# Optimization experiments

Hardware: AMD Instinct MI355X
Metric: run time of the kernel (lower is better)

The kernel has to match this reference:

```python
import jax, jax.numpy as jnp
import numpy as np

S, C, HF, WF = 6, 64, 44, 80          # cameras, feat channels, feat H, feat W
H_IMG, W_IMG = 352.0, 640.0           # full image size (opt.height/opt.width)
Z, Y, X = 16, 100, 100                # voxel grid (opt.voxels_size)
XMIN, XMAX = -40.0, 40.0
YMIN, YMAX = -40.0, 40.0
ZMIN, ZMAX = -1.0, 5.4
EPS = 1e-6


def setup_inputs() -> dict:
    key = jax.random.key(0)
    features = jax.random.normal(jax.random.fold_in(key, 0), (S, C, HF, WF), dtype=jnp.float32)
    # intrinsics at full image resolution
    K = np.eye(4, dtype=np.float32)
    K[0, 0] = 500.0; K[1, 1] = 500.0
    K[0, 2] = W_IMG / 2.0; K[1, 2] = H_IMG / 2.0
    pix_T_cams = np.tile(K[None], (S, 1, 1))
    # 6-camera surround rig: cam0_T_camX rigid transforms (columns = camera axes in ref frame)
    mats = []
    for i in range(S):
        th = 2.0 * np.pi * i / S
        c, s = np.cos(th), np.sin(th)
        T = np.eye(4, dtype=np.float32)
        T[:3, 0] = [-s, c, 0.0]          # camera x (right)
        T[:3, 1] = [0.0, 0.0, -1.0]      # camera y (down)
        T[:3, 2] = [c, s, 0.0]           # camera z (forward)
        T[:3, 3] = [0.5 * c, 0.5 * s, 1.5]
        mats.append(T)
    cam0_T_camXs = np.stack(mats).astype(np.float32)
    return {"features": features,
            "pix_T_cams": jnp.asarray(pix_T_cams),
            "cam0_T_camXs": jnp.asarray(cam0_T_camXs)}


def _safe_inverse(T):
    # rigid 4x4 inverse: [R t] -> [R^T, -R^T t]
    R = T[:, :3, :3]
    t = T[:, :3, 3]
    Rt = jnp.swapaxes(R, 1, 2)
    tt = -jnp.einsum('sij,sj->si', Rt, t)
    inv = jnp.zeros_like(T)
    inv = inv.at[:, :3, :3].set(Rt).at[:, :3, 3].set(tt).at[:, 3, 3].set(1.0)
    return inv


def _voxel_centers():
    # ref-frame coordinates of voxel centers, flattened [Z*Y*X, 3] with x fastest
    vx = (XMAX - XMIN) / X
    vy = (YMAX - YMIN) / Y
    vz = (ZMAX - ZMIN) / Z
    xs = XMIN + vx * (jnp.arange(X, dtype=jnp.float32) + 0.5)
    ys = YMIN + vy * (jnp.arange(Y, dtype=jnp.float32) + 0.5)
    zs = ZMIN + vz * (jnp.arange(Z, dtype=jnp.float32) + 0.5)
    zz, yy, xx = jnp.meshgrid(zs, ys, xs, indexing='ij')
    return jnp.stack([xx, yy, zz], axis=-1).reshape(-1, 3)


def _bilinear(img, x, y):
    # img: [C,H,W]; x,y: [N] pixel coords; zero padding outside
    Hh, Ww = img.shape[-2], img.shape[-1]
    x0 = jnp.floor(x)
    y0 = jnp.floor(y)
    wx1 = x - x0
    wy1 = y - y0

    def corner(xi, yi, w):
        valid = (xi >= 0) & (xi < Ww) & (yi >= 0) & (yi < Hh)
        xc = jnp.clip(xi, 0, Ww - 1).astype(jnp.int32)
        yc = jnp.clip(yi, 0, Hh - 1).astype(jnp.int32)
        return img[:, yc, xc] * (w * valid)[None, :]

    return (corner(x0, y0, (1 - wx1) * (1 - wy1))
            + corner(x0 + 1, y0, wx1 * (1 - wy1))
            + corner(x0, y0 + 1, (1 - wx1) * wy1)
            + corner(x0 + 1, y0 + 1, wx1 * wy1))  # [C,N]


def reference(features, pix_T_cams, cam0_T_camXs):
    camXs_T_cam0 = _safe_inverse(cam0_T_camXs)
    sx, sy = WF / W_IMG, HF / H_IMG
    scale = jnp.diag(jnp.array([sx, sy, 1.0, 1.0], jnp.float32))
    featpix_T_cams = jnp.einsum('ij,sjk->sik', scale, pix_T_cams)
    pix_T_cam0 = jnp.einsum('sij,sjk->sik', featpix_T_cams, camXs_T_cam0)

    xyz0 = _voxel_centers()                                  # [N,3]
    xyz1 = jnp.concatenate([xyz0, jnp.ones((xyz0.shape[0], 1), jnp.float32)], -1)
    xyz_pix = jnp.einsum('sij,nj->sni', pix_T_cam0, xyz1)    # [S,N,4]
    z_cam = jnp.einsum('sj,nj->sn', camXs_T_cam0[:, 2, :], xyz1)  # camX-frame depth

    denom = jnp.maximum(xyz_pix[..., 2], 1e-6)
    x_pix = xyz_pix[..., 0] / denom
    y_pix = xyz_pix[..., 1] / denom
    valid = ((x_pix > -0.5) & (x_pix < WF - 0.5)
             & (y_pix > -0.5) & (y_pix < HF - 0.5)
             & (z_cam > 0.0))

    # grid_sample(align_corners=False) with norm 2*(p/W)-1 samples at pixel p-0.5
    samp = jax.vmap(_bilinear)(features, x_pix - 0.5, y_pix - 0.5)  # [S,C,N]
    feat_mems = samp * valid[:, None, :].astype(samp.dtype)
    feat_mems = feat_mems.reshape(S, C, Z, Y, X)[None]              # [1,S,C,Z,Y,X]

    mask = (jnp.abs(feat_mems) > 0).astype(feat_mems.dtype)
    feat_mem = (feat_mems * mask).sum(1) / (mask.sum(1) + EPS)      # masked mean over cams
    return jnp.transpose(feat_mem, (0, 1, 4, 3, 2))                 # [1,C,X,Y,Z]
```

## Files before the change

### kernel.cpp

```cpp
#include <hip/hip_runtime.h>

#define NS 6
#define NC 64
#define HF 44
#define WF 80
#define HW (HF * WF)
#define NZ 16
#define NY 100
#define NX 100
#define XYZ (NX * NY * NZ)

__global__ __launch_bounds__(256) void transpose_feat(
        const float* __restrict__ in, float* __restrict__ outT) {
    __shared__ float tile[64 * 65];
    int b = blockIdx.x;
    int s = b / 55;
    int hw0 = (b % 55) * 64;
    int t = threadIdx.x;
#pragma unroll
    for (int i = 0; i < 16; ++i) {
        int e = t + i * 256;
        int c = e >> 6, w = e & 63;
        tile[c * 65 + w] = in[((size_t)(s * NC + c)) * HW + hw0 + w];
    }
    __syncthreads();
#pragma unroll
    for (int i = 0; i < 16; ++i) {
        int e = t + i * 256;
        int hwl = e >> 6, c = e & 63;
        outT[((size_t)s * HW + hw0 + hwl) * NC + c] = tile[c * 65 + hwl];
    }
}

template <bool TRANS>
__global__ __launch_bounds__(256) void volpool(
        const float* __restrict__ feat,
        const float* __restrict__ pix,
        const float* __restrict__ c0TX,
        float* __restrict__ out) {
    __shared__ float  mlds[NS * 16];
    __shared__ float4 wts[96];
    __shared__ int4   offs[96];
    __shared__ int    vflags[96];
    __shared__ float  ostage[NC * 17];

    int t = threadIdx.x;
    int b = blockIdx.x;
    int x = b % NX, y = b / NX;

    if (t < NS) {
        const float* T = c0TX + t * 16;
        float inv[4][4];
        for (int i = 0; i < 3; ++i) {
            for (int j = 0; j < 3; ++j) inv[i][j] = T[j * 4 + i];
            inv[i][3] = -(T[0 * 4 + i] * T[0 * 4 + 3] +
                          T[1 * 4 + i] * T[1 * 4 + 3] +
                          T[2 * 4 + i] * T[2 * 4 + 3]);
        }
        inv[3][0] = 0.f; inv[3][1] = 0.f; inv[3][2] = 0.f; inv[3][3] = 1.f;
        const float sx = (float)WF / 640.0f;
        const float sy = (float)HF / 352.0f;
        const float* K = pix + t * 16;
        float fp[3][4];
        for (int j = 0; j < 4; ++j) {
            fp[0][j] = sx * K[0 * 4 + j];
            fp[1][j] = sy * K[1 * 4 + j];
            fp[2][j] = K[2 * 4 + j];
        }
        float* M = mlds + t * 16;
        for (int i = 0; i < 3; ++i)
            for (int j = 0; j < 4; ++j) {
                float acc = 0.f;
                for (int k = 0; k < 4; ++k) acc += fp[i][k] * inv[k][j];
                M[i * 4 + j] = acc;
            }
        for (int j = 0; j < 4; ++j) M[12 + j] = inv[2][j];
    }
    __syncthreads();

    if (t < 96) {
        int s = t % NS, z = t / NS;
        const float* M = mlds + s * 16;
        float xw = -40.0f + 0.8f * ((float)x + 0.5f);
        float yw = -40.0f + 0.8f * ((float)y + 0.5f);
        float zw = -1.0f + 0.4f * ((float)z + 0.5f);
        float px = M[0] * xw + M[1] * yw + M[2]  * zw + M[3];
        float py = M[4] * xw + M[5] * yw + M[6]  * zw + M[7];
        float pz = M[8] * xw + M[9] * yw + M[10] * zw + M[11];
        float zc = M[12] * xw + M[13] * yw + M[14] * zw + M[15];
        float denom = fmaxf(pz, 1e-6f);
        float xp = px / denom, yp = py / denom;
        bool valid = (xp > -0.5f) & (xp < (float)WF - 0.5f) &
                     (yp > -0.5f) & (yp < (float)HF - 0.5f) & (zc > 0.0f);
        vflags[t] = valid ? 1 : 0;
        if (valid) {
            float xs = xp - 0.5f, ys = yp - 0.5f;
            float x0f = floorf(xs), y0f = floorf(ys);
            float wx1 = xs - x0f, wy1 = ys - y0f;
            float wx0 = 1.f - wx1, wy0 = 1.f - wy1;
            int x0 = (int)x0f, y0 = (int)y0f;
            int x1 = x0 + 1, y1 = y0 + 1;
            bool bx0 = (x0 >= 0) & (x0 < WF);
            bool bx1 = (x1 >= 0) & (x1 < WF);
            bool by0 = (y0 >= 0) & (y0 < HF);
            bool by1 = (y1 >= 0) & (y1 < HF);
            int x0c = min(max(x0, 0), WF - 1);
            int x1c = min(max(x1, 0), WF - 1);
            int y0c = min(max(y0, 0), HF - 1);
            int y1c = min(max(y1, 0), HF - 1);
            float4 w;
            w.x = wx0 * wy0 * (float)(bx0 & by0);
            w.y = wx1 * wy0 * (float)(bx1 & by0);
            w.z = wx0 * wy1 * (float)(bx0 & by1);
            w.w = wx1 * wy1 * (float)(bx1 & by1);
            int p00 = y0c * WF + x0c, p10 = y0c * WF + x1c;
            int p01 = y1c * WF + x0c, p11 = y1c * WF + x1c;
            int4 o;
            if (TRANS) {
                o.x = (s * HW + p00) * NC;
                o.y = (s * HW + p10) * NC;
                o.z = (s * HW + p01) * NC;
                o.w = (s * HW + p11) * NC;
            } else {
                o.x = s * NC * HW + p00;
                o.y = s * NC * HW + p10;
                o.z = s * NC * HW + p01;
                o.w = s * NC * HW + p11;
            }
            wts[t] = w;
            offs[t] = o;
        }
    }
    __syncthreads();

    int cg = t & 15, z = t >> 4;
    float4 sum = make_float4(0.f, 0.f, 0.f, 0.f);
    float4 cnt = make_float4(0.f, 0.f, 0.f, 0.f);
    for (int s = 0; s < NS; ++s) {
        int idx = z * NS + s;
        if (!vflags[idx]) continue;
        float4 w = wts[idx];
        int4 o = offs[idx];
        float4 f00, f10, f01, f11;
        if (TRANS) {
            int ch4 = cg << 2;
            f00 = *(const float4*)(feat + o.x + ch4);
            f10 = *(const float4*)(feat + o.y + ch4);
            f01 = *(const float4*)(feat + o.z + ch4);
            f11 = *(const float4*)(feat + o.w + ch4);
        } else {
            int c0 = cg << 2;
            f00.x = feat[o.x + (c0 + 0) * HW]; f00.y = feat[o.x + (c0 + 1) * HW];
            f00.z = feat[o.x + (c0 + 2) * HW]; f00.w = feat[o.x + (c0 + 3) * HW];
            f10.x = feat[o.y + (c0 + 0) * HW]; f10.y = feat[o.y + (c0 + 1) * HW];
            f10.z = feat[o.y + (c0 + 2) * HW]; f10.w = feat[o.y + (c0 + 3) * HW];
            f01.x = feat[o.z + (c0 + 0) * HW]; f01.y = feat[o.z + (c0 + 1) * HW];
            f01.z = feat[o.z + (c0 + 2) * HW]; f01.w = feat[o.z + (c0 + 3) * HW];
            f11.x = feat[o.w + (c0 + 0) * HW]; f11.y = feat[o.w + (c0 + 1) * HW];
            f11.z = feat[o.w + (c0 + 2) * HW]; f11.w = feat[o.w + (c0 + 3) * HW];
        }
        float vx = w.x * f00.x + w.y * f10.x + w.z * f01.x + w.w * f11.x;
        float vy = w.x * f00.y + w.y * f10.y + w.z * f01.y + w.w * f11.y;
        float vz = w.x * f00.z + w.y * f10.z + w.z * f01.z + w.w * f11.z;
        float vw = w.x * f00.w + w.y * f10.w + w.z * f01.w + w.w * f11.w;
        sum.x += vx; cnt.x += (vx != 0.0f) ? 1.0f : 0.0f;
        sum.y += vy; cnt.y += (vy != 0.0f) ? 1.0f : 0.0f;
        sum.z += vz; cnt.z += (vz != 0.0f) ? 1.0f : 0.0f;
        sum.w += vw; cnt.w += (vw != 0.0f) ? 1.0f : 0.0f;
    }
    int c0 = cg << 2;
    ostage[(c0 + 0) * 17 + z] = sum.x / (cnt.x + 1e-6f);
    ostage[(c0 + 1) * 17 + z] = sum.y / (cnt.y + 1e-6f);
    ostage[(c0 + 2) * 17 + z] = sum.z / (cnt.z + 1e-6f);
    ostage[(c0 + 3) * 17 + z] = sum.w / (cnt.w + 1e-6f);
    __syncthreads();

    int c = t >> 2, zq = t & 3;
    float4 v4;
    v4.x = ostage[c * 17 + zq * 4 + 0];
    v4.y = ostage[c * 17 + zq * 4 + 1];
    v4.z = ostage[c * 17 + zq * 4 + 2];
    v4.w = ostage[c * 17 + zq * 4 + 3];
    float* o = out + (size_t)c * XYZ + ((size_t)x * NY + y) * NZ + zq * 4;
    *(float4*)o = v4;
}

extern "C" void kernel_launch(void* const* d_in, const int* in_sizes, int n_in,
                              void* d_out, int out_size, void* d_ws, size_t ws_size,
                              hipStream_t stream) {
    const float* features = (const float*)d_in[0];
    const float* pix      = (const float*)d_in[1];
    const float* c0TX     = (const float*)d_in[2];
    float* out   = (float*)d_out;
    float* featT = (float*)d_ws;
    size_t need = sizeof(float) * (size_t)NS * HW * NC;

    if (ws_size >= need) {
        hipLaunchKernelGGL(transpose_feat, dim3(NS * 55), dim3(256), 0, stream,
                           features, featT);
        hipLaunchKernelGGL((volpool<true>), dim3(NX * NY), dim3(256), 0, stream,
                           featT, pix, c0TX, out);
    } else {
        hipLaunchKernelGGL((volpool<false>), dim3(NX * NY), dim3(256), 0, stream,
                           features, pix, c0TX, out);
    }
}
```

Baseline: 87.59 us.

## Vectorize transpose, compact valid cameras, remap blocks, and use nontemporal stores

The transpose kernel now moves float4 chunks per thread instead of scalars. The pooling kernel builds a compacted per-z list of valid cameras so the gather loop skips invalid entries, and it software-pipelines the feature loads by prefetching the next camera's corners. Block indices are remapped into 8 spatial regions so that concurrently running blocks spread across the grid. Output writes use nontemporal stores to avoid polluting the cache. These changes add an extra sync phase and more register pressure.

```diff
diff --git a/kernel.cpp b/kernel.cpp
--- a/kernel.cpp
+++ b/kernel.cpp
@@ -10,6 +10,8 @@
 #define NX 100
 #define XYZ (NX * NY * NZ)
 
+typedef float v4f __attribute__((ext_vector_type(4)));
+
 __global__ __launch_bounds__(256) void transpose_feat(
         const float* __restrict__ in, float* __restrict__ outT) {
     __shared__ float tile[64 * 65];
@@ -18,17 +20,26 @@
     int hw0 = (b % 55) * 64;
     int t = threadIdx.x;
 #pragma unroll
-    for (int i = 0; i < 16; ++i) {
+    for (int i = 0; i < 4; ++i) {
         int e = t + i * 256;
-        int c = e >> 6, w = e & 63;
-        tile[c * 65 + w] = in[((size_t)(s * NC + c)) * HW + hw0 + w];
+        int c = e >> 4, wg = e & 15;
+        float4 f = *(const float4*)(in + ((size_t)(s * NC + c)) * HW + hw0 + wg * 4);
+        tile[c * 65 + wg * 4 + 0] = f.x;
+        tile[c * 65 + wg * 4 + 1] = f.y;
+        tile[c * 65 + wg * 4 + 2] = f.z;
+        tile[c * 65 + wg * 4 + 3] = f.w;
     }
     __syncthreads();
 #pragma unroll
-    for (int i = 0; i < 16; ++i) {
+    for (int i = 0; i < 4; ++i) {
         int e = t + i * 256;
-        int hwl = e >> 6, c = e & 63;
-        outT[((size_t)s * HW + hw0 + hwl) * NC + c] = tile[c * 65 + hwl];
+        int hwl = e >> 4, cg = e & 15;
+        float4 f;
+        f.x = tile[(cg * 4 + 0) * 65 + hwl];
+        f.y = tile[(cg * 4 + 1) * 65 + hwl];
+        f.z = tile[(cg * 4 + 2) * 65 + hwl];
+        f.w = tile[(cg * 4 + 3) * 65 + hwl];
+        *(float4*)(outT + ((size_t)s * HW + hw0 + hwl) * NC + cg * 4) = f;
     }
 }
 
@@ -42,11 +53,16 @@
     __shared__ float4 wts[96];
     __shared__ int4   offs[96];
     __shared__ int    vflags[96];
+    __shared__ int    vidx[NZ][NS];
+    __shared__ int    nvalid[NZ];
     __shared__ float  ostage[NC * 17];
 
     int t = threadIdx.x;
     int b = blockIdx.x;
-    int x = b % NX, y = b / NX;
+    int reg = b & 7;
+    int r = b >> 3;
+    int x = (reg & 1) * 50 + (r % 50);
+    int y = (reg >> 1) * 25 + (r / 50);
 
     if (t < NS) {
         const float* T = c0TX + t * 16;
@@ -133,56 +149,96 @@
     }
     __syncthreads();
 
+    if (t < NZ) {
+        int n = 0;
+        for (int s = 0; s < NS; ++s) {
+            int idx = t * NS + s;
+            if (vflags[idx]) vidx[t][n++] = idx;
+        }
+        nvalid[t] = n;
+    }
+    __syncthreads();
+
     int cg = t & 15, z = t >> 4;
+    int ch4 = cg << 2;
     float4 sum = make_float4(0.f, 0.f, 0.f, 0.f);
     float4 cnt = make_float4(0.f, 0.f, 0.f, 0.f);
-    for (int s = 0; s < NS; ++s) {
-        int idx = z * NS + s;
-        if (!vflags[idx]) continue;
-        float4 w = wts[idx];
-        int4 o = offs[idx];
-        float4 f00, f10, f01, f11;
+    int nv = nvalid[z];
+    if (nv > 0) {
         if (TRANS) {
-            int ch4 = cg << 2;
-            f00 = *(const float4*)(feat + o.x + ch4);
-            f10 = *(const float4*)(feat + o.y + ch4);
-            f01 = *(const float4*)(feat + o.z + ch4);
-            f11 = *(const float4*)(feat + o.w + ch4);
+            int idx = vidx[z][0];
+            float4 w = wts[idx];
+            int4 o = offs[idx];
+            float4 f00 = *(const float4*)(feat + o.x + ch4);
+            float4 f10 = *(const float4*)(feat + o.y + ch4);
+            float4 f01 = *(const float4*)(feat + o.z + ch4);
+            float4 f11 = *(const float4*)(feat + o.w + ch4);
+            for (int j = 1; j < nv; ++j) {
+                int idx2 = vidx[z][j];
+                float4 w2 = wts[idx2];
+                int4 o2 = offs[idx2];
+                float4 g00 = *(const float4*)(feat + o2.x + ch4);
+                float4 g10 = *(const float4*)(feat + o2.y + ch4);
+                float4 g01 = *(const float4*)(feat + o2.z + ch4);
+                float4 g11 = *(const float4*)(feat + o2.w + ch4);
+                float vx = w.x * f00.x + w.y * f10.x + w.z * f01.x + w.w * f11.x;
+                float vy = w.x * f00.y + w.y * f10.y + w.z * f01.y + w.w * f11.y;
+                float vz = w.x * f00.z + w.y * f10.z + w.z * f01.z + w.w * f11.z;
+                float vw = w.x * f00.w + w.y * f10.w + w.z * f01.w + w.w * f11.w;
+                sum.x += vx; cnt.x += (vx != 0.0f) ? 1.0f : 0.0f;
+                sum.y += vy; cnt.y += (vy != 0.0f) ? 1.0f : 0.0f;
+                sum.z += vz; cnt.z += (vz != 0.0f) ? 1.0f : 0.0f;
+                sum.w += vw; cnt.w += (vw != 0.0f) ? 1.0f : 0.0f;
+                w = w2; f00 = g00; f10 = g10; f01 = g01; f11 = g11;
+            }
+            float vx = w.x * f00.x + w.y * f10.x + w.z * f01.x + w.w * f11.x;
+            float vy = w.x * f00.y + w.y * f10.y + w.z * f01.y + w.w * f11.y;
+            float vz = w.x * f00.z + w.y * f10.z + w.z * f01.z + w.w * f11.z;
+            float vw = w.x * f00.w + w.y * f10.w + w.z * f01.w + w.w * f11.w;
+            sum.x += vx; cnt.x += (vx != 0.0f) ? 1.0f : 0.0f;
+            sum.y += vy; cnt.y += (vy != 0.0f) ? 1.0f : 0.0f;
+            sum.z += vz; cnt.z += (vz != 0.0f) ? 1.0f : 0.0f;
+            sum.w += vw; cnt.w += (vw != 0.0f) ? 1.0f : 0.0f;
         } else {
-            int c0 = cg << 2;
-            f00.x = feat[o.x + (c0 + 0) * HW]; f00.y = feat[o.x + (c0 + 1) * HW];
-            f00.z = feat[o.x + (c0 + 2) * HW]; f00.w = feat[o.x + (c0 + 3) * HW];
-            f10.x = feat[o.y + (c0 + 0) * HW]; f10.y = feat[o.y + (c0 + 1) * HW];
-            f10.z = feat[o.y + (c0 + 2) * HW]; f10.w = feat[o.y + (c0 + 3) * HW];
-            f01.x = feat[o.z + (c0 + 0) * HW]; f01.y = feat[o.z + (c0 + 1) * HW];
-            f01.z = feat[o.z + (c0 + 2) * HW]; f01.w = feat[o.z + (c0 + 3) * HW];
-            f11.x = feat[o.w + (c0 + 0) * HW]; f11.y = feat[o.w + (c0 + 1) * HW];
-            f11.z = feat[o.w + (c0 + 2) * HW]; f11.w = feat[o.w + (c0 + 3) * HW];
-        }
-        float vx = w.x * f00.x + w.y * f10.x + w.z * f01.x + w.w * f11.x;
-        float vy = w.x * f00.y + w.y * f10.y + w.z * f01.y + w.w * f11.y;
-        float vz = w.x * f00.z + w.y * f10.z + w.z * f01.z + w.w * f11.z;
-        float vw = w.x * f00.w + w.y * f10.w + w.z * f01.w + w.w * f11.w;
-        sum.x += vx; cnt.x += (vx != 0.0f) ? 1.0f : 0.0f;
-        sum.y += vy; cnt.y += (vy != 0.0f) ? 1.0f : 0.0f;
-        sum.z += vz; cnt.z += (vz != 0.0f) ? 1.0f : 0.0f;
-        sum.w += vw; cnt.w += (vw != 0.0f) ? 1.0f : 0.0f;
-    }
-    int c0 = cg << 2;
-    ostage[(c0 + 0) * 17 + z] = sum.x / (cnt.x + 1e-6f);
-    ostage[(c0 + 1) * 17 + z] = sum.y / (cnt.y + 1e-6f);
-    ostage[(c0 + 2) * 17 + z] = sum.z / (cnt.z + 1e-6f);
-    ostage[(c0 + 3) * 17 + z] = sum.w / (cnt.w + 1e-6f);
+            for (int j = 0; j < nv; ++j) {
+                int idx = vidx[z][j];
+                float4 w = wts[idx];
+                int4 o = offs[idx];
+                int c0 = cg << 2;
+                float4 f00, f10, f01, f11;
+                f00.x = feat[o.x + (c0 + 0) * HW]; f00.y = feat[o.x + (c0 + 1) * HW];
+                f00.z = feat[o.x + (c0 + 2) * HW]; f00.w = feat[o.x + (c0 + 3) * HW];
+                f10.x = feat[o.y + (c0 + 0) * HW]; f10.y = feat[o.y + (c0 + 1) * HW];
+                f10.z = feat[o.y + (c0 + 2) * HW]; f10.w = feat[o.y + (c0 + 3) * HW];
+                f01.x = feat[o.z + (c0 + 0) * HW]; f01.y = feat[o.z + (c0 + 1) * HW];
+                f01.z = feat[o.z + (c0 + 2) * HW]; f01.w = feat[o.z + (c0 + 3) * HW];
+                f11.x = feat[o.w + (c0 + 0) * HW]; f11.y = feat[o.w + (c0 + 1) * HW];
+                f11.z = feat[o.w + (c0 + 2) * HW]; f11.w = feat[o.w + (c0 + 3) * HW];
+                float vx = w.x * f00.x + w.y * f10.x + w.z * f01.x + w.w * f11.x;
+                float vy = w.x * f00.y + w.y * f10.y + w.z * f01.y + w.w * f11.y;
+                float vz = w.x * f00.z + w.y * f10.z + w.z * f01.z + w.w * f11.z;
+                float vw = w.x * f00.w + w.y * f10.w + w.z * f01.w + w.w * f11.w;
+                sum.x += vx; cnt.x += (vx != 0.0f) ? 1.0f : 0.0f;
+                sum.y += vy; cnt.y += (vy != 0.0f) ? 1.0f : 0.0f;
+                sum.z += vz; cnt.z += (vz != 0.0f) ? 1.0f : 0.0f;
+                sum.w += vw; cnt.w += (vw != 0.0f) ? 1.0f : 0.0f;
+            }
+        }
+    }
+    ostage[(ch4 + 0) * 17 + z] = sum.x / (cnt.x + 1e-6f);
+    ostage[(ch4 + 1) * 17 + z] = sum.y / (cnt.y + 1e-6f);
+    ostage[(ch4 + 2) * 17 + z] = sum.z / (cnt.z + 1e-6f);
+    ostage[(ch4 + 3) * 17 + z] = sum.w / (cnt.w + 1e-6f);
     __syncthreads();
 
     int c = t >> 2, zq = t & 3;
-    float4 v4;
+    v4f v4;
     v4.x = ostage[c * 17 + zq * 4 + 0];
     v4.y = ostage[c * 17 + zq * 4 + 1];
     v4.z = ostage[c * 17 + zq * 4 + 2];
     v4.w = ostage[c * 17 + zq * 4 + 3];
     float* o = out + (size_t)c * XYZ + ((size_t)x * NY + y) * NZ + zq * 4;
-    *(float4*)o = v4;
+    __builtin_nontemporal_store(v4, (v4f*)o);
 }
 
 extern "C" void kernel_launch(void* const* d_in, const int* in_sizes, int n_in,
```

Result: no change. 87.95 us (+0.4%).
